# Kernel optimization log

Measured on AMD Instinct MI355X. Metric: run time of the kernel, lower is better.

The kernel has to match this reference:

```python
import jax, jax.numpy as jnp
import numpy as np

D_MODEL = 256
KSIZE = 16
EPS = 1e-5


def conv1d(x, w, b):
    # x: [B, C, N], w: [O, C, K], SAME padding over node axis
    y = jax.lax.conv_general_dilated(x, w, window_strides=(1,), padding='SAME',
                                     dimension_numbers=('NCH', 'OIH', 'NCH'))
    return y + b[None, :, None]


def layernorm(x, g, b):
    mu = jnp.mean(x, axis=-1, keepdims=True)
    var = jnp.mean(jnp.square(x - mu), axis=-1, keepdims=True)
    return (x - mu) * jax.lax.rsqrt(var + EPS) * g + b


def setup_inputs() -> dict:
    key = jax.random.key(0)
    ks = jax.random.split(key, 16)
    B, N, d, K = 4, 2048, D_MODEL, KSIZE
    conv_scale = 1.0 / np.sqrt(d * K)
    lin_scale = 1.0 / np.sqrt(d)
    return {
        'src': jax.random.normal(ks[0], (B, N, d), jnp.float32),
        'x_lst': jnp.zeros((B, N, N), jnp.float32),
        'adj': jax.random.randint(ks[1], (B, N, N), 0, 2, jnp.int32),
        'dis': jax.random.uniform(ks[2], (B, N, N), jnp.float32),
        'Wq': jax.random.normal(ks[3], (d, d, K), jnp.float32) * conv_scale,
        'bq': jnp.zeros((d,), jnp.float32),
        'Wk': jax.random.normal(ks[4], (d, d, K), jnp.float32) * conv_scale,
        'bk': jnp.zeros((d,), jnp.float32),
        'Wv': jax.random.normal(ks[5], (d, d, K), jnp.float32) * conv_scale,
        'bv': jnp.zeros((d,), jnp.float32),
        'W1': jax.random.normal(ks[6], (d, d), jnp.float32) * lin_scale,
        'b1': jnp.zeros((d,), jnp.float32),
        'W2': jax.random.normal(ks[7], (d, d), jnp.float32) * lin_scale,
        'b2': jnp.zeros((d,), jnp.float32),
        'W3': jax.random.normal(ks[8], (d, d), jnp.float32) * lin_scale,
        'b3': jnp.zeros((d,), jnp.float32),
        'g1': jnp.ones((d,), jnp.float32),
        'be1': jnp.zeros((d,), jnp.float32),
        'g2': jnp.ones((d,), jnp.float32),
        'be2': jnp.zeros((d,), jnp.float32),
    }


def reference(src, x_lst, adj, dis, Wq, bq, Wk, bk, Wv, bv,
              W1, b1, W2, b2, W3, b3, g1, be1, g2, be2):
    # ---- _ga_block: transpose to channel-major, graph attention ----
    x = jnp.swapaxes(src, -2, -1)                      # [B, d, N]
    q = conv1d(x, Wq, bq)                              # [B, d, N]
    k = conv1d(x, Wk, bk)
    v = conv1d(x, Wv, bv)
    scale = 1.0 / jnp.sqrt(jnp.asarray(D_MODEL, src.dtype))
    scores = jnp.einsum('bdn,bdm->bnm', q, k) * scale  # [B, N, N]
    scores = scores - dis                              # distance bias
    scores = jnp.where(adj > 0, scores, jnp.asarray(-1e9, scores.dtype))
    attn = jax.nn.softmax(scores, axis=-1)             # [B, N, N]
    x_lst_new = x_lst + attn                           # accumulated attention state
    out = jnp.einsum('bnm,bdm->bdn', attn, v)          # [B, d, N]
    x1 = jnp.swapaxes(out, -2, -1)                     # [B, N, d] (dropout = identity in eval)
    # ---- residual + norm1 ----
    h = layernorm(src + x1, g1, be1)
    # ---- 3-layer LeakyReLU MLP + residual + norm2 ----
    m = jax.nn.leaky_relu(h @ W1.T + b1)
    m = jax.nn.leaky_relu(m @ W2.T + b2)
    m = m @ W3.T + b3
    h = layernorm(h + m, g2, be2)
    return h, x_lst_new
```

## Files before the change

kernel.cpp:

```cpp
#include <hip/hip_runtime.h>
#include <stdint.h>

typedef _Float16 h16;
typedef _Float16 h4v __attribute__((ext_vector_type(4)));
typedef _Float16 h8v __attribute__((ext_vector_type(8)));
typedef float    f4v __attribute__((ext_vector_type(4)));
typedef int      i4v __attribute__((ext_vector_type(4)));

#define NBATCH 4
#define NNODE  2048
#define DM     256
#define NPAD   2063
#define QKELEM 2097152
#define PARTN  (8192 * 256)

__device__ __forceinline__ void async16(const void* g, void* l) {
#if __has_builtin(__builtin_amdgcn_global_load_lds)
  __builtin_amdgcn_global_load_lds((__attribute__((address_space(1))) void*)g,
                                   (__attribute__((address_space(3))) void*)l, 16, 0, 0);
#else
  *(f4v*)l = *(const f4v*)g;
#endif
}

__device__ __forceinline__ void gemm_tile(
    const h16* Abase, int astride,
    const h16* Bbase, int bstride,
    h16* As, h16* Bs, f4v acc[4][4], int kiters)
{
  const int tid  = threadIdx.x;
  const int lane = tid & 63;
  const int wv   = tid >> 6;
  const int srow = tid >> 2;
  const int sch  = ((tid & 3) ^ ((tid >> 3) & 3)) * 8;
  const h16* gA0 = Abase + (long)srow * astride + sch;
  const h16* gA1 = Abase + (long)(srow + 64) * astride + sch;
  const h16* gB0 = Bbase + (long)srow * bstride + sch;
  const h16* gB1 = Bbase + (long)(srow + 64) * bstride + sch;
  h16* lA0 = As + tid * 8;
  h16* lA1 = As + 2048 + tid * 8;
  h16* lB0 = Bs + tid * 8;
  h16* lB1 = Bs + 2048 + tid * 8;
  const int swz = ((lane & 15) >> 1) & 3;
  const int qq  = ((lane >> 4) ^ swz) * 8;
  const int amr = ((wv & 1) * 64 + (lane & 15)) * 32 + qq;
  const int bnr = ((wv >> 1) * 64 + (lane & 15)) * 32 + qq;

  for (int kt = 0; kt < kiters; ++kt) {
    const int k0 = kt * 32;
    __syncthreads();
    async16(gA0 + k0, lA0);
    async16(gA1 + k0, lA1);
    async16(gB0 + k0, lB0);
    async16(gB1 + k0, lB1);
    asm volatile("s_waitcnt vmcnt(0)" ::: "memory");
    __syncthreads();
    h8v af[4], bf[4];
#pragma unroll
    for (int i = 0; i < 4; ++i) af[i] = *(const h8v*)(As + amr + i * 512);
#pragma unroll
    for (int j = 0; j < 4; ++j) bf[j] = *(const h8v*)(Bs + bnr + j * 512);
#pragma unroll
    for (int i = 0; i < 4; ++i)
#pragma unroll
      for (int j = 0; j < 4; ++j)
        acc[i][j] = __builtin_amdgcn_mfma_f32_16x16x32_f16(af[i], bf[j], acc[i][j], 0, 0, 0);
  }
}

__device__ __forceinline__ void zero_acc(f4v acc[4][4]) {
#pragma unroll
  for (int i = 0; i < 4; ++i)
#pragma unroll
    for (int j = 0; j < 4; ++j) {
      f4v z = {0.f, 0.f, 0.f, 0.f};
      acc[i][j] = z;
    }
}

#define NSRC_BLK 8252
__global__ __launch_bounds__(256) void prep_all_kernel(
    const float* __restrict__ src,
    const float* __restrict__ Wq, const float* __restrict__ Wk, const float* __restrict__ Wv,
    const float* __restrict__ W1, const float* __restrict__ W2, const float* __restrict__ W3,
    h16* __restrict__ Xpad, h16* __restrict__ Wt, h16* __restrict__ Wl)
{
  __shared__ float plds[16][257];
  const int bi = blockIdx.x, tid = threadIdx.x;
  if (bi < NSRC_BLK) {
    int idx = bi * 256 + tid;
    int c = idx & 255;
    int row = idx >> 8;
    int b = row / NPAD;
    int n = row - b * NPAD;
    float v = 0.f;
    int ns = n - 7;
    if (ns >= 0 && ns < NNODE) v = src[((long)b * NNODE + ns) * DM + c];
    Xpad[idx] = (h16)v;
  } else if (bi < NSRC_BLK + 768) {
    const int q = bi - NSRC_BLK;
    const int w = q >> 8, o = q & 255;
    const float* W = (w == 0) ? Wq : (w == 1) ? Wk : Wv;
    const float* base = W + (long)o * 4096;
    f4v r0 = *(const f4v*)(base + tid * 16);
    f4v r1 = *(const f4v*)(base + tid * 16 + 4);
    f4v r2 = *(const f4v*)(base + tid * 16 + 8);
    f4v r3 = *(const f4v*)(base + tid * 16 + 12);
#pragma unroll
    for (int k = 0; k < 4; ++k) {
      plds[k][tid] = r0[k]; plds[4 + k][tid] = r1[k];
      plds[8 + k][tid] = r2[k]; plds[12 + k][tid] = r3[k];
    }
    __syncthreads();
    const int t = tid >> 4, c0 = (tid & 15) * 16;
    h16* out = Wt + ((long)(w * 256 + o)) * 4096 + t * 256 + c0;
    h8v o0, o1;
#pragma unroll
    for (int k = 0; k < 8; ++k) { o0[k] = (h16)plds[t][c0 + k]; o1[k] = (h16)plds[t][c0 + 8 + k]; }
    *(h8v*)out = o0;
    *(h8v*)(out + 8) = o1;
  } else {
    int idx = (bi - NSRC_BLK - 768) * 256 + tid;
    int w = idx >> 16;
    int rem = idx & 65535;
    const float* W = (w == 0) ? W1 : (w == 1) ? W2 : W3;
    Wl[idx] = (h16)W[rem];
  }
}

__global__ __launch_bounds__(256) void conv_gemm_kernel(
    const h16* __restrict__ Xpad, const h16* __restrict__ Wt,
    h16* __restrict__ Qp, h16* __restrict__ Kp, h16* __restrict__ Vp)
{
  __shared__ __align__(16) h16 As[4096];
  __shared__ __align__(16) h16 Bs[4096];
  const int mt = blockIdx.x, ct = blockIdx.y;
  const int w = blockIdx.z >> 2, ks = blockIdx.z & 3;
  const int m0 = mt * 128;
  const int b = m0 >> 11, n0 = m0 & 2047;
  const h16* Abase = Xpad + ((long)(b * NPAD + n0)) * DM + ks * 1024;
  const h16* Bbase = Wt + (long)w * (256 * 4096) + (long)ct * 128 * 4096 + ks * 1024;
  f4v acc[4][4];
  zero_acc(acc);
  gemm_tile(Abase, DM, Bbase, 4096, As, Bs, acc, 32);

  h16* dst = ((w == 0) ? Qp : (w == 1) ? Kp : Vp) + (long)ks * QKELEM;
  const int lane = threadIdx.x & 63, wv = threadIdx.x >> 6;
  const int rbase = (wv & 1) * 64 + (lane >> 4) * 4;
  const int cbase = (wv >> 1) * 64 + (lane & 15);
#pragma unroll
  for (int j = 0; j < 4; ++j) {
    const int gc = ct * 128 + cbase + j * 16;
#pragma unroll
    for (int i = 0; i < 4; ++i) {
#pragma unroll
      for (int e = 0; e < 4; ++e) {
        const int gr = m0 + rbase + i * 16 + e;
        const h16 v = (h16)acc[i][j][e];
        if (w == 2) {
          const int bb = gr >> 11, n = gr & 2047;
          dst[((long)(bb * 256 + gc)) * 2048 + n] = v;
        } else {
          dst[(long)gr * 256 + gc] = v;
        }
      }
    }
  }
}

__global__ __launch_bounds__(256) void conv_reduce_kernel(
    const h16* __restrict__ Qp, const h16* __restrict__ Kp, const h16* __restrict__ Vp,
    const float* __restrict__ bq, const float* __restrict__ bk, const float* __restrict__ bv,
    h16* __restrict__ Qb, h16* __restrict__ Kb, h16* __restrict__ Vt)
{
  const long gid = (long)blockIdx.x * 256 + threadIdx.x;
  if (gid < 2 * (QKELEM / 8)) {
    const int which = gid >= (QKELEM / 8);
    const long e = (gid - (long)which * (QKELEM / 8)) * 8;
    const h16* P = which ? Kp : Qp;
    const float* bias = which ? bk : bq;
    float s[8] = {0.f, 0.f, 0.f, 0.f, 0.f, 0.f, 0.f, 0.f};
#pragma unroll
    for (int ks = 0; ks < 4; ++ks) {
      h8v p = *(const h8v*)(P + (long)ks * QKELEM + e);
#pragma unroll
      for (int k = 0; k < 8; ++k) s[k] += (float)p[k];
    }
    const int c0 = (int)(e & 255);
    h8v o;
#pragma unroll
    for (int k = 0; k < 8; ++k) o[k] = (h16)(s[k] + bias[c0 + k]);
    *(h8v*)((which ? Kb : Qb) + e) = o;
  } else {
    const long e = (gid - 2 * (QKELEM / 8)) * 8;
    float s[8] = {0.f, 0.f, 0.f, 0.f, 0.f, 0.f, 0.f, 0.f};
#pragma unroll
    for (int ks = 0; ks < 4; ++ks) {
      h8v p = *(const h8v*)(Vp + (long)ks * QKELEM + e);
#pragma unroll
      for (int k = 0; k < 8; ++k) s[k] += (float)p[k];
    }
    const float bias_v = bv[(int)((e >> 11) & 255)];
    h8v o;
#pragma unroll
    for (int k = 0; k < 8; ++k) o[k] = (h16)(s[k] + bias_v);
    *(h8v*)(Vt + e) = o;
  }
}

__global__ __launch_bounds__(256) void scores_gemm_kernel(
    const h16* __restrict__ Q, const h16* __restrict__ Km, h16* __restrict__ Sh)
{
  __shared__ __align__(16) h16 As[4096];
  __shared__ __align__(16) h16 Bs[4096];
  const int nt = blockIdx.x, mt = blockIdx.y, b = blockIdx.z;
  const h16* Abase = Q + ((long)b * NNODE + nt * 128) * 256;
  const h16* Bbase = Km + ((long)b * NNODE + mt * 128) * 256;
  f4v acc[4][4];
  zero_acc(acc);
  gemm_tile(Abase, 256, Bbase, 256, As, Bs, acc, 8);

  const int lane = threadIdx.x & 63, wv = threadIdx.x >> 6;
  const int rbase = (wv & 1) * 64 + (lane >> 4) * 4;
  const int cbase = (wv >> 1) * 64 + (lane & 15);
  h16* Srow = Sh + (long)b * NNODE * NNODE;
#pragma unroll
  for (int i = 0; i < 4; ++i) {
#pragma unroll
    for (int e = 0; e < 4; ++e) {
      const long row = nt * 128 + rbase + i * 16 + e;
#pragma unroll
      for (int j = 0; j < 4; ++j) {
        const int col = mt * 128 + cbase + j * 16;
        Srow[row * 2048 + col] = (h16)(acc[i][j][e] * 0.0625f);
      }
    }
  }
}

__device__ __forceinline__ float wred_max(float v) {
#pragma unroll
  for (int off = 32; off > 0; off >>= 1) v = fmaxf(v, __shfl_xor(v, off, 64));
  return v;
}
__device__ __forceinline__ float wred_sum(float v) {
#pragma unroll
  for (int off = 32; off > 0; off >>= 1) v += __shfl_xor(v, off, 64);
  return v;
}

__global__ __launch_bounds__(256) void softmax_kernel(
    h16* __restrict__ Sh, const float* __restrict__ dis, const int* __restrict__ adj,
    const float* __restrict__ x_lst, float* __restrict__ out_x)
{
  const int r = blockIdx.x;
  const long ro = (long)r * 2048;
  const int tid = threadIdx.x, lane = tid & 63, wv = tid >> 6;
  const int j0 = tid * 8;
  __shared__ float wmax[4], wsum[4];

  h8v sv = *(const h8v*)(Sh + ro + j0);
  f4v d0 = *(const f4v*)(dis + ro + j0);
  f4v d1 = *(const f4v*)(dis + ro + j0 + 4);
  i4v a0 = *(const i4v*)(adj + ro + j0);
  i4v a1 = *(const i4v*)(adj + ro + j0 + 4);

  float s[8];
#pragma unroll
  for (int k = 0; k < 4; ++k) s[k]     = (a0[k] > 0) ? ((float)sv[k]     - d0[k]) : -1e9f;
#pragma unroll
  for (int k = 0; k < 4; ++k) s[k + 4] = (a1[k] > 0) ? ((float)sv[k + 4] - d1[k]) : -1e9f;

  float m = s[0];
#pragma unroll
  for (int k = 1; k < 8; ++k) m = fmaxf(m, s[k]);
  m = wred_max(m);
  if (lane == 0) wmax[wv] = m;
  __syncthreads();
  m = fmaxf(fmaxf(wmax[0], wmax[1]), fmaxf(wmax[2], wmax[3]));

  float p[8], ls = 0.f;
#pragma unroll
  for (int k = 0; k < 8; ++k) { p[k] = __expf(s[k] - m); ls += p[k]; }
  ls = wred_sum(ls);
  if (lane == 0) wsum[wv] = ls;
  __syncthreads();
  const float inv = 1.0f / (wsum[0] + wsum[1] + wsum[2] + wsum[3]);

  f4v x0 = *(const f4v*)(x_lst + ro + j0);
  f4v x1 = *(const f4v*)(x_lst + ro + j0 + 4);
  f4v o0, o1;
  h8v pv;
#pragma unroll
  for (int k = 0; k < 4; ++k) {
    const float a = p[k] * inv, bq = p[k + 4] * inv;
    o0[k] = x0[k] + a; o1[k] = x1[k] + bq;
    pv[k] = (h16)a; pv[k + 4] = (h16)bq;
  }
  *(f4v*)(out_x + ro + j0) = o0;
  *(f4v*)(out_x + ro + j0 + 4) = o1;
  *(h8v*)(Sh + ro + j0) = pv;
}

__global__ __launch_bounds__(256) void av_gemm_kernel(
    const h16* __restrict__ Attn, const h16* __restrict__ Vt, h16* __restrict__ X1p)
{
  __shared__ __align__(16) h16 As[4096];
  __shared__ __align__(16) h16 Bs[4096];
  const int nt = blockIdx.x, b = blockIdx.z;
  const int ct = blockIdx.y & 1, ks = blockIdx.y >> 1;
  const h16* Abase = Attn + ((long)b * NNODE + nt * 128) * 2048 + ks * 1024;
  const h16* Bbase = Vt + ((long)b * 256 + ct * 128) * 2048 + ks * 1024;
  f4v acc[4][4];
  zero_acc(acc);
  gemm_tile(Abase, 2048, Bbase, 2048, As, Bs, acc, 32);

  const int lane = threadIdx.x & 63, wv = threadIdx.x >> 6;
  const int rbase = (wv & 1) * 64 + (lane >> 4) * 4;
  const int cbase = (wv >> 1) * 64 + (lane & 15);
  h16* dst = X1p + (long)ks * PARTN;
#pragma unroll
  for (int i = 0; i < 4; ++i) {
#pragma unroll
    for (int e = 0; e < 4; ++e) {
      const long row = (long)b * NNODE + nt * 128 + rbase + i * 16 + e;
#pragma unroll
      for (int j = 0; j < 4; ++j) {
        const int col = ct * 128 + cbase + j * 16;
        dst[row * 256 + col] = (h16)acc[i][j][e];
      }
    }
  }
}

__global__ __launch_bounds__(256) void ln1_kernel(
    const float* __restrict__ X, const h16* __restrict__ Y, const h16* __restrict__ Y2,
    const float* __restrict__ g, const float* __restrict__ bb,
    float* __restrict__ outF, h16* __restrict__ outH)
{
  const int wv = threadIdx.x >> 6, lane = threadIdx.x & 63;
  const long r = (long)blockIdx.x * 4 + wv;
  const long off = r * 256 + lane * 4;
  f4v x = *(const f4v*)(X + off);
  h4v y = *(const h4v*)(Y + off);
  h4v y2 = *(const h4v*)(Y2 + off);
  float v[4];
  float sum = 0.f, sq = 0.f;
#pragma unroll
  for (int k = 0; k < 4; ++k) {
    v[k] = x[k] + (float)y[k] + (float)y2[k];
    sum += v[k]; sq += v[k] * v[k];
  }
  sum = wred_sum(sum);
  sq  = wred_sum(sq);
  const float mu = sum * (1.0f / 256.0f);
  const float var = sq * (1.0f / 256.0f) - mu * mu;
  const float rs = rsqrtf(var + 1e-5f);
  f4v gg = *(const f4v*)(g + lane * 4);
  f4v be = *(const f4v*)(bb + lane * 4);
  f4v o;
#pragma unroll
  for (int k = 0; k < 4; ++k) o[k] = (v[k] - mu) * rs * gg[k] + be[k];
  *(f4v*)(outF + off) = o;
  h4v hv;
#pragma unroll
  for (int k = 0; k < 4; ++k) hv[k] = (h16)o[k];
  *(h4v*)(outH + off) = hv;
}

__global__ __launch_bounds__(256) void mlp_fused_kernel(
    const h16* __restrict__ H16, const float* __restrict__ Hf,
    const h16* __restrict__ Wl,
    const float* __restrict__ b1, const float* __restrict__ b2, const float* __restrict__ b3,
    const float* __restrict__ g2, const float* __restrict__ be2,
    float* __restrict__ out_h)
{
  __shared__ h16 Xa[32][264];
  __shared__ h16 Xb[32][264];
  __shared__ __align__(16) h16 Bs[8192];
  const int tid = threadIdx.x, lane = tid & 63, wv = tid >> 6;
  const int m0 = blockIdx.x * 32;

  {
    const int r = tid >> 3, cq = (tid & 7) * 32;
    const h16* s = H16 + (long)(m0 + r) * 256 + cq;
#pragma unroll
    for (int k = 0; k < 4; ++k)
      *(h8v*)&Xa[r][cq + k * 8] = *(const h8v*)(s + k * 8);
  }

  const int srow = tid >> 2;
  const int sch  = ((tid & 3) ^ ((tid >> 3) & 3)) * 8;
  h16* lB = Bs + tid * 8;
  const int quad = lane >> 4;
  const float* biases[3] = {b1, b2, b3};

  for (int layer = 0; layer < 3; ++layer) {
    const h16* W = Wl + layer * 65536;
    const h16 (*Xi)[264] = (layer == 1) ? (const h16(*)[264])Xb : (const h16(*)[264])Xa;
    h16 (*Xo)[264] = (layer == 1) ? Xa : Xb;
    f4v acc[2][4];
#pragma unroll
    for (int i = 0; i < 2; ++i)
#pragma unroll
      for (int j = 0; j < 4; ++j) { f4v z = {0.f,0.f,0.f,0.f}; acc[i][j] = z; }

    for (int kt = 0; kt < 8; ++kt) {
      __syncthreads();
      const h16* gB = W + (long)srow * 256 + kt * 32 + sch;
      async16(gB, lB);
      async16(gB + 64 * 256, lB + 64 * 32);
      async16(gB + 128 * 256, lB + 128 * 32);
      async16(gB + 192 * 256, lB + 192 * 32);
      asm volatile("s_waitcnt vmcnt(0)" ::: "memory");
      __syncthreads();
      h8v af[2], bf[4];
#pragma unroll
      for (int i = 0; i < 2; ++i)
        af[i] = *(const h8v*)&Xi[i * 16 + (lane & 15)][kt * 32 + quad * 8];
#pragma unroll
      for (int j = 0; j < 4; ++j) {
        const int n = wv * 64 + j * 16 + (lane & 15);
        const int q = (quad ^ ((n >> 1) & 3)) * 8;
        bf[j] = *(const h8v*)(Bs + n * 32 + q);
      }
#pragma unroll
      for (int i = 0; i < 2; ++i)
#pragma unroll
        for (int j = 0; j < 4; ++j)
          acc[i][j] = __builtin_amdgcn_mfma_f32_16x16x32_f16(af[i], bf[j], acc[i][j], 0, 0, 0);
    }
    const int rb = quad * 4;
    const int cb = wv * 64 + (lane & 15);
    const float* bias = biases[layer];
    const bool leaky = (layer < 2);
#pragma unroll
    for (int j = 0; j < 4; ++j) {
      const int col = cb + j * 16;
      const float bv = bias[col];
#pragma unroll
      for (int i = 0; i < 2; ++i)
#pragma unroll
        for (int e = 0; e < 4; ++e) {
          float v = acc[i][j][e] + bv;
          if (leaky) v = (v >= 0.f) ? v : 0.01f * v;
          Xo[i * 16 + rb + e][col] = (h16)v;
        }
    }
  }
  __syncthreads();

  const int r = tid >> 3, c0 = (tid & 7) * 32;
  const float* hrow = Hf + (long)(m0 + r) * 256 + c0;
  float v[32];
  float s = 0.f, sq = 0.f;
#pragma unroll
  for (int k8 = 0; k8 < 8; ++k8) {
    f4v h4 = *(const f4v*)(hrow + k8 * 4);
#pragma unroll
    for (int e = 0; e < 4; ++e) {
      float t = (float)Xb[r][c0 + k8 * 4 + e] + h4[e];
      v[k8 * 4 + e] = t; s += t; sq += t * t;
    }
  }
#pragma unroll
  for (int off = 1; off < 8; off <<= 1) { s += __shfl_xor(s, off, 64); sq += __shfl_xor(sq, off, 64); }
  const float mu = s * (1.0f / 256.0f);
  const float var = sq * (1.0f / 256.0f) - mu * mu;
  const float rs = rsqrtf(var + 1e-5f);
  float* orow = out_h + (long)(m0 + r) * 256 + c0;
#pragma unroll
  for (int k8 = 0; k8 < 8; ++k8) {
    f4v gg = *(const f4v*)(g2 + c0 + k8 * 4);
    f4v be = *(const f4v*)(be2 + c0 + k8 * 4);
    f4v o;
#pragma unroll
    for (int e = 0; e < 4; ++e) o[e] = (v[k8 * 4 + e] - mu) * rs * gg[e] + be[e];
    *(f4v*)(orow + k8 * 4) = o;
  }
}

extern "C" void kernel_launch(void* const* d_in, const int* in_sizes, int n_in,
                              void* d_out, int out_size, void* d_ws, size_t ws_size,
                              hipStream_t stream)
{
  const float* src  = (const float*)d_in[0];
  const float* xlst = (const float*)d_in[1];
  const int*   adj  = (const int*)d_in[2];
  const float* dis  = (const float*)d_in[3];
  const float* Wq   = (const float*)d_in[4];
  const float* bq   = (const float*)d_in[5];
  const float* Wk   = (const float*)d_in[6];
  const float* bk   = (const float*)d_in[7];
  const float* Wv   = (const float*)d_in[8];
  const float* bvp  = (const float*)d_in[9];
  const float* W1   = (const float*)d_in[10];
  const float* b1   = (const float*)d_in[11];
  const float* W2   = (const float*)d_in[12];
  const float* b2   = (const float*)d_in[13];
  const float* W3   = (const float*)d_in[14];
  const float* b3   = (const float*)d_in[15];
  const float* g1   = (const float*)d_in[16];
  const float* be1  = (const float*)d_in[17];
  const float* g2   = (const float*)d_in[18];
  const float* be2  = (const float*)d_in[19];
  (void)in_sizes; (void)n_in; (void)out_size; (void)ws_size;

  char* ws = (char*)d_ws;
  size_t off = 0;
  auto alloc = [&](size_t bytes) -> void* {
    void* p = ws + off;
    off += (bytes + 1023) & ~(size_t)1023;
    return p;
  };
  h16*   Xpad = (h16*)  alloc((size_t)NBATCH * NPAD * DM * 2);
  h16*   Wt   = (h16*)  alloc((size_t)3 * 256 * 4096 * 2);
  h16*   Wl   = (h16*)  alloc((size_t)3 * 256 * 256 * 2);
  h16*   Qb   = (h16*)  alloc((size_t)QKELEM * 2);
  h16*   Kb   = (h16*)  alloc((size_t)QKELEM * 2);
  h16*   Vt   = (h16*)  alloc((size_t)QKELEM * 2);
  char*  R    = (char*) alloc((size_t)66000 * 1024);
  h16*   Qp   = (h16*)R;
  h16*   Kp   = (h16*)(R + (size_t)4 * QKELEM * 2);
  h16*   Vp   = (h16*)(R + (size_t)8 * QKELEM * 2);
  h16*   Sh   = (h16*)R;
  h16*   X1p  = Vp;
  float* H    = (float*)(R + (size_t)12 * QKELEM * 2);
  h16*   H16  = (h16*)((char*)H + (size_t)PARTN * 4);

  float* out_h = (float*)d_out;
  float* out_x = out_h + (size_t)NBATCH * NNODE * DM;

  prep_all_kernel<<<NSRC_BLK + 768 + 768, 256, 0, stream>>>(
      src, Wq, Wk, Wv, W1, W2, W3, Xpad, Wt, Wl);
  conv_gemm_kernel<<<dim3(64, 2, 12), 256, 0, stream>>>(Xpad, Wt, Qp, Kp, Vp);
  conv_reduce_kernel<<<3 * (QKELEM / 8) / 256, 256, 0, stream>>>(
      Qp, Kp, Vp, bq, bk, bvp, Qb, Kb, Vt);
  scores_gemm_kernel<<<dim3(16, 16, 4), 256, 0, stream>>>(Qb, Kb, Sh);
  softmax_kernel<<<NBATCH * NNODE, 256, 0, stream>>>(Sh, dis, adj, xlst, out_x);
  av_gemm_kernel<<<dim3(16, 4, 4), 256, 0, stream>>>(Sh, Vt, X1p);
  ln1_kernel<<<(NBATCH * NNODE) / 4, 256, 0, stream>>>(src, X1p, X1p + PARTN, g1, be1, H, H16);
  mlp_fused_kernel<<<NBATCH * NNODE / 32, 256, 0, stream>>>(
      H16, H, Wl, b1, b2, b3, g2, be2, out_h);
}
```

Measured before the change: 446.2 us.

## Use 256x256 double-buffered conv GEMM tiles with 2-way split-K and LDS transpose reduce

Replaces the 128x128 conv GEMM (4-way split-K, 768 blocks) with a 512-thread 256x256 tile kernel. It runs a 64-deep K step with double-buffered LDS, interleaves async loads between MFMA quarters, and raises wave priority with s_setprio. Split-K drops from 4 to 2, so the partial buffers and the reduce traffic are halved. The V transpose moves out of scattered GEMM stores into an LDS-transposed pass inside the reduce kernel. The grid is only 192 blocks and each block uses 128KB of LDS, which lowers occupancy and may leave CUs idle.

Result: faster. 417.8 us (-6.4%).

```diff
diff --git a/kernel.cpp b/kernel.cpp
--- a/kernel.cpp
+++ b/kernel.cpp
@@ -22,6 +22,9 @@
   *(f4v*)l = *(const f4v*)g;
 #endif
 }
+
+#define BARRIER() do { asm volatile("" ::: "memory"); __builtin_amdgcn_s_barrier(); asm volatile("" ::: "memory"); } while (0)
+#define MFMA16 __builtin_amdgcn_mfma_f32_16x16x32_f16
 
 __device__ __forceinline__ void gemm_tile(
     const h16* Abase, int astride,
@@ -64,7 +67,7 @@
     for (int i = 0; i < 4; ++i)
 #pragma unroll
       for (int j = 0; j < 4; ++j)
-        acc[i][j] = __builtin_amdgcn_mfma_f32_16x16x32_f16(af[i], bf[j], acc[i][j], 0, 0, 0);
+        acc[i][j] = MFMA16(af[i], bf[j], acc[i][j], 0, 0, 0);
   }
 }
 
@@ -128,44 +131,155 @@
   }
 }
 
-__global__ __launch_bounds__(256) void conv_gemm_kernel(
+__global__ __launch_bounds__(512) void conv_gemm256_kernel(
     const h16* __restrict__ Xpad, const h16* __restrict__ Wt,
     h16* __restrict__ Qp, h16* __restrict__ Kp, h16* __restrict__ Vp)
 {
-  __shared__ __align__(16) h16 As[4096];
-  __shared__ __align__(16) h16 Bs[4096];
-  const int mt = blockIdx.x, ct = blockIdx.y;
-  const int w = blockIdx.z >> 2, ks = blockIdx.z & 3;
-  const int m0 = mt * 128;
-  const int b = m0 >> 11, n0 = m0 & 2047;
-  const h16* Abase = Xpad + ((long)(b * NPAD + n0)) * DM + ks * 1024;
-  const h16* Bbase = Wt + (long)w * (256 * 4096) + (long)ct * 128 * 4096 + ks * 1024;
-  f4v acc[4][4];
-  zero_acc(acc);
-  gemm_tile(Abase, DM, Bbase, 4096, As, Bs, acc, 32);
+  __shared__ __align__(16) h16 As[32768];
+  __shared__ __align__(16) h16 Bs[32768];
+  const int tid  = threadIdx.x;
+  const int lane = tid & 63, wv = tid >> 6;
+  const int mt = blockIdx.x, w = blockIdx.y, ks = blockIdx.z;
+  const int m0 = mt * 256;
+  const int b  = m0 >> 11, n0 = m0 & 2047;
+
+  const int rh = tid >> 3;
+  const int cs = (((tid & 7) ^ ((tid >> 3) & 7)) << 3);
+  const h16* AgT = Xpad + ((long)(b * NPAD + n0) << 8) + ((long)ks << 11) + (long)rh * 256 + cs;
+  const h16* BgT = Wt + ((long)w << 20) + ((long)ks << 11) + (long)rh * 4096 + cs;
+  h16* lA = As + tid * 8;
+  h16* lB = Bs + tid * 8;
+
+  auto stageA = [&](int kt, int half) {
+    h16* d = lA + ((kt & 1) << 14) + (half << 13);
+    const h16* g = AgT + half * (128 * 256) + kt * 64;
+    async16(g, d);
+    async16(g + 64 * 256, d + 4096);
+  };
+  auto stageB = [&](int kt, int half) {
+    h16* d = lB + ((kt & 1) << 14) + (half << 13);
+    const h16* g = BgT + half * (128 * 4096) + kt * 64;
+    async16(g, d);
+    async16(g + 64 * 4096, d + 4096);
+  };
+
+  const int wr = wv >> 2, wc = wv & 3;
+  const int e0 = (((lane >> 4) ^ (lane & 7)) << 3);
+  const int e1 = e0 ^ 32;
+  const h16* pA0 = As + (wr * 128 + (lane & 15)) * 64 + e0;
+  const h16* pA1 = pA0 + (e1 - e0);
+  const h16* pB0 = Bs + (wc * 64 + (lane & 15)) * 64 + e0;
+  const h16* pB1 = pB0 + (e1 - e0);
+
+  f4v acc[8][4];
+#pragma unroll
+  for (int i = 0; i < 8; ++i)
+#pragma unroll
+    for (int j = 0; j < 4; ++j) { f4v z = {0.f, 0.f, 0.f, 0.f}; acc[i][j] = z; }
+
+  stageA(0, 0); stageA(0, 1); stageB(0, 0); stageB(0, 1); stageA(1, 0);
+  asm volatile("s_waitcnt vmcnt(2)" ::: "memory");
+  BARRIER();
+
+#pragma unroll 1
+  for (int kt = 0; kt < 32; ++kt) {
+    const int sb = (kt & 1) << 14;
+    h8v ar[4][2], bL[2][2], bR[2][2];
+#pragma unroll
+    for (int i = 0; i < 4; ++i) {
+      ar[i][0] = *(const h8v*)(pA0 + sb + i * 1024);
+      ar[i][1] = *(const h8v*)(pA1 + sb + i * 1024);
+    }
+#pragma unroll
+    for (int j = 0; j < 2; ++j) {
+      bL[j][0] = *(const h8v*)(pB0 + sb + j * 1024);
+      bL[j][1] = *(const h8v*)(pB1 + sb + j * 1024);
+    }
+    if (kt < 31) stageA(kt + 1, 1);
+    BARRIER();
+    __builtin_amdgcn_s_setprio(1);
+#pragma unroll
+    for (int i = 0; i < 4; ++i)
+#pragma unroll
+      for (int j = 0; j < 2; ++j) {
+        acc[i][j] = MFMA16(ar[i][0], bL[j][0], acc[i][j], 0, 0, 0);
+        acc[i][j] = MFMA16(ar[i][1], bL[j][1], acc[i][j], 0, 0, 0);
+      }
+    __builtin_amdgcn_s_setprio(0);
+    BARRIER();
+#pragma unroll
+    for (int j = 0; j < 2; ++j) {
+      bR[j][0] = *(const h8v*)(pB0 + sb + (j + 2) * 1024);
+      bR[j][1] = *(const h8v*)(pB1 + sb + (j + 2) * 1024);
+    }
+    if (kt < 31) stageB(kt + 1, 0);
+    BARRIER();
+    __builtin_amdgcn_s_setprio(1);
+#pragma unroll
+    for (int i = 0; i < 4; ++i)
+#pragma unroll
+      for (int j = 0; j < 2; ++j) {
+        acc[i][j + 2] = MFMA16(ar[i][0], bR[j][0], acc[i][j + 2], 0, 0, 0);
+        acc[i][j + 2] = MFMA16(ar[i][1], bR[j][1], acc[i][j + 2], 0, 0, 0);
+      }
+    __builtin_amdgcn_s_setprio(0);
+    BARRIER();
+#pragma unroll
+    for (int i = 0; i < 4; ++i) {
+      ar[i][0] = *(const h8v*)(pA0 + sb + (i + 4) * 1024);
+      ar[i][1] = *(const h8v*)(pA1 + sb + (i + 4) * 1024);
+    }
+    if (kt < 31) stageB(kt + 1, 1);
+    BARRIER();
+    __builtin_amdgcn_s_setprio(1);
+#pragma unroll
+    for (int i = 0; i < 4; ++i)
+#pragma unroll
+      for (int j = 0; j < 2; ++j) {
+        acc[i + 4][j + 2] = MFMA16(ar[i][0], bR[j][0], acc[i + 4][j + 2], 0, 0, 0);
+        acc[i + 4][j + 2] = MFMA16(ar[i][1], bR[j][1], acc[i + 4][j + 2], 0, 0, 0);
+      }
+    __builtin_amdgcn_s_setprio(0);
+    BARRIER();
+#pragma unroll
+    for (int j = 0; j < 2; ++j) {
+      bL[j][0] = *(const h8v*)(pB0 + sb + j * 1024);
+      bL[j][1] = *(const h8v*)(pB1 + sb + j * 1024);
+    }
+    if (kt < 30) {
+      stageA(kt + 2, 0);
+      asm volatile("s_waitcnt vmcnt(2)" ::: "memory");
+    } else if (kt == 30) {
+      asm volatile("s_waitcnt vmcnt(0)" ::: "memory");
+    }
+    BARRIER();
+    __builtin_amdgcn_s_setprio(1);
+#pragma unroll
+    for (int i = 0; i < 4; ++i)
+#pragma unroll
+      for (int j = 0; j < 2; ++j) {
+        acc[i + 4][j] = MFMA16(ar[i][0], bL[j][0], acc[i + 4][j], 0, 0, 0);
+        acc[i + 4][j] = MFMA16(ar[i][1], bL[j][1], acc[i + 4][j], 0, 0, 0);
+      }
+    __builtin_amdgcn_s_setprio(0);
+    BARRIER();
+  }
 
   h16* dst = ((w == 0) ? Qp : (w == 1) ? Kp : Vp) + (long)ks * QKELEM;
-  const int lane = threadIdx.x & 63, wv = threadIdx.x >> 6;
-  const int rbase = (wv & 1) * 64 + (lane >> 4) * 4;
-  const int cbase = (wv >> 1) * 64 + (lane & 15);
-#pragma unroll
-  for (int j = 0; j < 4; ++j) {
-    const int gc = ct * 128 + cbase + j * 16;
-#pragma unroll
-    for (int i = 0; i < 4; ++i) {
+  const int rb = (lane >> 4) * 4;
+  const int cb = wc * 64 + (lane & 15);
+  const int mrow0 = m0 + wr * 128;
+#pragma unroll
+  for (int i = 0; i < 8; ++i)
+#pragma unroll
+    for (int j = 0; j < 4; ++j) {
+      const int gc = cb + j * 16;
 #pragma unroll
       for (int e = 0; e < 4; ++e) {
-        const int gr = m0 + rbase + i * 16 + e;
-        const h16 v = (h16)acc[i][j][e];
-        if (w == 2) {
-          const int bb = gr >> 11, n = gr & 2047;
-          dst[((long)(bb * 256 + gc)) * 2048 + n] = v;
-        } else {
-          dst[(long)gr * 256 + gc] = v;
-        }
-      }
-    }
-  }
+        const int gr = mrow0 + i * 16 + rb + e;
+        dst[(long)gr * 256 + gc] = (h16)acc[i][j][e];
+      }
+    }
 }
 
 __global__ __launch_bounds__(256) void conv_reduce_kernel(
@@ -173,38 +287,46 @@
     const float* __restrict__ bq, const float* __restrict__ bk, const float* __restrict__ bv,
     h16* __restrict__ Qb, h16* __restrict__ Kb, h16* __restrict__ Vt)
 {
-  const long gid = (long)blockIdx.x * 256 + threadIdx.x;
-  if (gid < 2 * (QKELEM / 8)) {
+  __shared__ float T[64][65];
+  const int bi = blockIdx.x, tid = threadIdx.x;
+  if (bi < 2048) {
+    const long gid = (long)bi * 256 + tid;
     const int which = gid >= (QKELEM / 8);
     const long e = (gid - (long)which * (QKELEM / 8)) * 8;
     const h16* P = which ? Kp : Qp;
     const float* bias = which ? bk : bq;
-    float s[8] = {0.f, 0.f, 0.f, 0.f, 0.f, 0.f, 0.f, 0.f};
-#pragma unroll
-    for (int ks = 0; ks < 4; ++ks) {
-      h8v p = *(const h8v*)(P + (long)ks * QKELEM + e);
-#pragma unroll
-      for (int k = 0; k < 8; ++k) s[k] += (float)p[k];
-    }
+    h8v p0 = *(const h8v*)(P + e);
+    h8v p1 = *(const h8v*)(P + QKELEM + e);
     const int c0 = (int)(e & 255);
     h8v o;
 #pragma unroll
-    for (int k = 0; k < 8; ++k) o[k] = (h16)(s[k] + bias[c0 + k]);
+    for (int k = 0; k < 8; ++k) o[k] = (h16)((float)p0[k] + (float)p1[k] + bias[c0 + k]);
     *(h8v*)((which ? Kb : Qb) + e) = o;
   } else {
-    const long e = (gid - 2 * (QKELEM / 8)) * 8;
-    float s[8] = {0.f, 0.f, 0.f, 0.f, 0.f, 0.f, 0.f, 0.f};
-#pragma unroll
-    for (int ks = 0; ks < 4; ++ks) {
-      h8v p = *(const h8v*)(Vp + (long)ks * QKELEM + e);
-#pragma unroll
-      for (int k = 0; k < 8; ++k) s[k] += (float)p[k];
-    }
-    const float bias_v = bv[(int)((e >> 11) & 255)];
-    h8v o;
-#pragma unroll
-    for (int k = 0; k < 8; ++k) o[k] = (h16)(s[k] + bias_v);
-    *(h8v*)(Vt + e) = o;
+    const int q = bi - 2048;
+    const int mt = q >> 2, ct = q & 3;
+    const int m0 = mt * 64, c0 = ct * 64;
+    const int b = m0 >> 11, n0 = m0 & 2047;
+    const int rr = tid >> 3, cc = (tid & 7) * 8;
+#pragma unroll
+    for (int p = 0; p < 2; ++p) {
+      const int r = p * 32 + rr;
+      const long so = (long)(m0 + r) * 256 + c0 + cc;
+      h8v p0 = *(const h8v*)(Vp + so);
+      h8v p1 = *(const h8v*)(Vp + QKELEM + so);
+#pragma unroll
+      for (int e = 0; e < 8; ++e) T[r][cc + e] = (float)p0[e] + (float)p1[e];
+    }
+    __syncthreads();
+#pragma unroll
+    for (int p = 0; p < 2; ++p) {
+      const int d = p * 32 + rr;
+      const float bias_v = bv[c0 + d];
+      h8v o;
+#pragma unroll
+      for (int e = 0; e < 8; ++e) o[e] = (h16)(T[cc + e][d] + bias_v);
+      *(h8v*)(Vt + ((long)(b * 256 + c0 + d)) * 2048 + n0 + cc) = o;
+    }
   }
 }
 
@@ -428,7 +550,7 @@
       for (int i = 0; i < 2; ++i)
 #pragma unroll
         for (int j = 0; j < 4; ++j)
-          acc[i][j] = __builtin_amdgcn_mfma_f32_16x16x32_f16(af[i], bf[j], acc[i][j], 0, 0, 0);
+          acc[i][j] = MFMA16(af[i], bf[j], acc[i][j], 0, 0, 0);
     }
     const int rb = quad * 4;
     const int cb = wv * 64 + (lane & 15);
@@ -521,10 +643,10 @@
   h16*   Vt   = (h16*)  alloc((size_t)QKELEM * 2);
   char*  R    = (char*) alloc((size_t)66000 * 1024);
   h16*   Qp   = (h16*)R;
-  h16*   Kp   = (h16*)(R + (size_t)4 * QKELEM * 2);
-  h16*   Vp   = (h16*)(R + (size_t)8 * QKELEM * 2);
+  h16*   Kp   = (h16*)(R + (size_t)2 * QKELEM * 2);
+  h16*   Vp   = (h16*)(R + (size_t)4 * QKELEM * 2);
   h16*   Sh   = (h16*)R;
-  h16*   X1p  = Vp;
+  h16*   X1p  = (h16*)(R + (size_t)8 * QKELEM * 2);
   float* H    = (float*)(R + (size_t)12 * QKELEM * 2);
   h16*   H16  = (h16*)((char*)H + (size_t)PARTN * 4);
 
@@ -533,8 +655,8 @@
 
   prep_all_kernel<<<NSRC_BLK + 768 + 768, 256, 0, stream>>>(
       src, Wq, Wk, Wv, W1, W2, W3, Xpad, Wt, Wl);
-  conv_gemm_kernel<<<dim3(64, 2, 12), 256, 0, stream>>>(Xpad, Wt, Qp, Kp, Vp);
-  conv_reduce_kernel<<<3 * (QKELEM / 8) / 256, 256, 0, stream>>>(
+  conv_gemm256_kernel<<<dim3(32, 3, 2), 512, 0, stream>>>(Xpad, Wt, Qp, Kp, Vp);
+  conv_reduce_kernel<<<2048 + 512, 256, 0, stream>>>(
       Qp, Kp, Vp, bq, bk, bvp, Qb, Kb, Vt);
   scores_gemm_kernel<<<dim3(16, 16, 4), 256, 0, stream>>>(Qb, Kb, Sh);
   softmax_kernel<<<NBATCH * NNODE, 256, 0, stream>>>(Sh, dis, adj, xlst, out_x);
```
